# Kernel tuning notes

Hardware: AMD Instinct MI355X
Metric: run time of the kernel (lower is better)

Reference implementation:

```python
import jax, jax.numpy as jnp
import numpy as np
import math

EMBD_SIZE = 1024
OUT_SIZE = 1024
B, N = 8, 2048

def setup_inputs() -> dict:
    key = jax.random.key(0)
    k1, k2, k3 = jax.random.split(key, 3)
    embd = jax.random.normal(k1, (B, N, EMBD_SIZE), dtype=jnp.float32)
    # nn.Linear(embd_size, out_size): weight [out, in], bias [out]
    bound = 1.0 / math.sqrt(EMBD_SIZE)
    W = jax.random.uniform(k2, (OUT_SIZE, EMBD_SIZE), dtype=jnp.float32, minval=-bound, maxval=bound)
    b = jax.random.uniform(k3, (OUT_SIZE,), dtype=jnp.float32, minval=-bound, maxval=bound)
    return {"embd": embd, "W": W, "b": b}

def reference(embd, W, b):
    # c = Linear(embd): [B, N, out_size]
    c = jnp.einsum('bne,oe->bno', embd, W) + b
    # scores = c @ c^T / sqrt(embd_size), softmax over last dim
    score = jnp.einsum('bno,bmo->bnm', c, c) / jnp.sqrt(jnp.float32(EMBD_SIZE))
    score = jax.nn.softmax(score, axis=-1)
    # output = score @ c : [B, N, out_size]
    return jnp.einsum('bnm,bmo->bno', score, c)
```

## Files before the change

### kernel.cpp

```cpp
#include <hip/hip_runtime.h>

typedef unsigned short u16;
typedef unsigned int u32;
typedef __attribute__((ext_vector_type(8))) short short8;
typedef __attribute__((ext_vector_type(4))) float f32x4;

__device__ inline u16 f2bf(float f) {
  u32 x = __float_as_uint(f);
  x += 0x7fff + ((x >> 16) & 1);
  return (u16)(x >> 16);
}
__device__ inline float bf2f(u16 h) {
  return __uint_as_float(((u32)h) << 16);
}
__device__ inline void gload16(const void* g, void* l) {
  __builtin_amdgcn_global_load_lds((const __attribute__((address_space(1))) u32*)g,
                                   (__attribute__((address_space(3))) u32*)l, 16, 0, 0);
}

__device__ inline int sg(int r) {
  return ((r >> 3) & 7) ^ (((r >> 2) & 1) << 2) ^ (((r >> 3) & 1) << 1);
}
__device__ inline int stile_off(int rl, int cl) {
  return rl * 128 + (((cl >> 3) ^ sg(rl)) << 3) + (cl & 7);
}

__global__ void cast_all(const float* __restrict__ embd, const float* __restrict__ W,
                         u16* __restrict__ embd_b, u16* __restrict__ W_b) {
  const float* src; u16* dst; size_t i;
  if (blockIdx.x < 16384) {
    src = embd; dst = embd_b;
    i = ((size_t)blockIdx.x * 256 + threadIdx.x) * 4;
  } else {
    src = W; dst = W_b;
    i = ((size_t)(blockIdx.x - 16384) * 256 + threadIdx.x) * 4;
  }
  float4 v = *(const float4*)(src + i);
  ushort4 o;
  o.x = f2bf(v.x); o.y = f2bf(v.y); o.z = f2bf(v.z); o.w = f2bf(v.w);
  *(ushort4*)(dst + i) = o;
}

#define BM 128
#define BN 128
#define BK 64

template<int MODE>
__global__ __launch_bounds__(256, 2)
void gemm_nt(const u16* __restrict__ A, const u16* __restrict__ B,
             float* __restrict__ Cf, u16* __restrict__ Cb, u16* __restrict__ CT,
             const float* __restrict__ bias, float* __restrict__ rowsum,
             int M, int N, int K, float scale, long sA, long sB, long sC)
{
  __shared__ __align__(16) char smem[32768];
  u16* As = (u16*)smem;
  u16* Bs = As + BM * BK;
  u16* stile = (u16*)smem;
  float* stf = (float*)smem;

  int z, mBase, nBase, bi = 0, bj = 0;
  if (MODE == 0) {
    z = 0;
    mBase = blockIdx.y * BM;
    nBase = blockIdx.x * BN;
  } else if (MODE == 1) {
    z = blockIdx.x;
    int t = blockIdx.y, row = 0;
    const int nb = N >> 7;
    while (t >= nb - row) { t -= nb - row; ++row; }
    bi = row; bj = row + t;
    mBase = bi * BM; nBase = bj * BN;
  } else {
    z = blockIdx.x;
    nBase = (blockIdx.y & 7) * BN;
    mBase = (blockIdx.y >> 3) * BM;
  }

  A += (size_t)z * sA;
  B += (size_t)z * sB;
  if (MODE == 2) Cf += (size_t)z * sC; else Cb += (size_t)z * sC;
  if (MODE != 0) rowsum += (size_t)z * M;

  const int tid  = threadIdx.x;
  const int lane = tid & 63;
  const int wave = tid >> 6;
  const int wm = (wave >> 1) * 64;
  const int wn = (wave & 1) * 64;
  const int q = lane >> 4;
  const int r = lane & 15;
  const int rswz = r & 7;

  const int srow = tid >> 3;
  const int scol = ((tid & 7) ^ (srow & 7)) * 8;
  const int lds0 = tid * 16;

  const u16* a0 = A + (size_t)(mBase + srow) * K + scol;
  const u16* b0 = B + (size_t)(nBase + srow) * K + scol;

  f32x4 acc[4][4] = {};

  for (int k0 = 0; k0 < K; k0 += BK) {
#pragma unroll
    for (int i = 0; i < 4; ++i)
      gload16(a0 + (size_t)(32 * i) * K + k0, (char*)As + lds0 + i * 4096);
#pragma unroll
    for (int i = 0; i < 4; ++i)
      gload16(b0 + (size_t)(32 * i) * K + k0, (char*)Bs + lds0 + i * 4096);
    __syncthreads();

#pragma unroll
    for (int kk = 0; kk < 2; ++kk) {
      short8 af[4], bfr[4];
#pragma unroll
      for (int t = 0; t < 4; ++t) {
        const int go = (((kk * 4 + q) ^ rswz)) * 8;
        af[t]  = *(const short8*)(As + (wm + t * 16 + r) * BK + go);
        bfr[t] = *(const short8*)(Bs + (wn + t * 16 + r) * BK + go);
      }
#pragma unroll
      for (int mi = 0; mi < 4; ++mi)
#pragma unroll
        for (int ni = 0; ni < 4; ++ni)
          acc[mi][ni] = __builtin_amdgcn_mfma_f32_16x16x32_bf16(af[mi], bfr[ni], acc[mi][ni], 0, 0, 0);
    }
    __syncthreads();
  }


  if (MODE == 0) {
    float bv[4];
#pragma unroll
    for (int ni = 0; ni < 4; ++ni) bv[ni] = bias[nBase + wn + ni * 16 + r];
#pragma unroll
    for (int mi = 0; mi < 4; ++mi)
#pragma unroll
      for (int ni = 0; ni < 4; ++ni)
#pragma unroll
        for (int reg = 0; reg < 4; ++reg) {
          int rl = wm + mi * 16 + q * 4 + reg;
          int cl = wn + ni * 16 + r;
          stile[stile_off(rl, cl)] = f2bf(acc[mi][ni][reg] + bv[ni]);
        }
    __syncthreads();
    {
      const int z1 = mBase >> 11;
      const int n0 = mBase & 2047;
      u16* ctb = CT + (size_t)z1 * 1024 * 2048;
#pragma unroll
      for (int rnd = 0; rnd < 8; ++rnd) {
        int idx = rnd * 256 + tid;
        int ch = idx & 15, n = idx >> 4;
        short8 v = *(const short8*)(stile + n * 128 + ((ch ^ sg(n)) << 3));
        *(short8*)(Cb + (size_t)(mBase + n) * N + nBase + ch * 8) = v;
      }
#pragma unroll
      for (int rnd = 0; rnd < 8; ++rnd) {
        int idx = rnd * 256 + tid;
        int ch = idx & 15, cc = idx >> 4;
        short8 v;
#pragma unroll
        for (int j = 0; j < 8; ++j) v[j] = (short)stile[stile_off(ch * 8 + j, cc)];
        *(short8*)(ctb + (size_t)(nBase + cc) * 2048 + n0 + ch * 8) = v;
      }
    }
  } else if (MODE == 1) {
    const bool mirror = (bi != bj);
    float colacc[4] = {0.f, 0.f, 0.f, 0.f};
#pragma unroll
    for (int mi = 0; mi < 4; ++mi) {
      float rs[4] = {0.f, 0.f, 0.f, 0.f};
#pragma unroll
      for (int ni = 0; ni < 4; ++ni)
#pragma unroll
        for (int reg = 0; reg < 4; ++reg) {
          float e = __expf(acc[mi][ni][reg] * scale);
          u16 h = f2bf(e);
          float f = bf2f(h);
          rs[reg] += f;
          if (mirror) colacc[ni] += f;
          stile[stile_off(wm + mi * 16 + q * 4 + reg, wn + ni * 16 + r)] = h;
        }
#pragma unroll
      for (int reg = 0; reg < 4; ++reg) {
        float v = rs[reg];
        v += __shfl_xor(v, 1);
        v += __shfl_xor(v, 2);
        v += __shfl_xor(v, 4);
        v += __shfl_xor(v, 8);
        if (r == 0)
          atomicAdd(&rowsum[mBase + wm + mi * 16 + q * 4 + reg], v);
      }
    }
    if (mirror) {
#pragma unroll
      for (int ni = 0; ni < 4; ++ni) {
        float v = colacc[ni];
        v += __shfl_xor(v, 16);
        v += __shfl_xor(v, 32);
        if (q == 0)
          atomicAdd(&rowsum[nBase + wn + ni * 16 + r], v);
      }
    }
    __syncthreads();
#pragma unroll
    for (int rnd = 0; rnd < 8; ++rnd) {
      int idx = rnd * 256 + tid;
      int ch = idx & 15, n = idx >> 4;
      short8 v = *(const short8*)(stile + n * 128 + ((ch ^ sg(n)) << 3));
      *(short8*)(Cb + (size_t)(mBase + n) * N + nBase + ch * 8) = v;
    }
    if (mirror) {
#pragma unroll
      for (int rnd = 0; rnd < 8; ++rnd) {
        int idx = rnd * 256 + tid;
        int ch = idx & 15, cc = idx >> 4;
        short8 v;
#pragma unroll
        for (int j = 0; j < 8; ++j) v[j] = (short)stile[stile_off(ch * 8 + j, cc)];
        *(short8*)(Cb + (size_t)(nBase + cc) * N + mBase + ch * 8) = v;
      }
    }
  } else {
#pragma unroll
    for (int p = 0; p < 2; ++p) {
      if ((wave >> 1) == p) {
#pragma unroll
        for (int mi = 0; mi < 4; ++mi)
#pragma unroll
          for (int reg = 0; reg < 4; ++reg) {
            int lr = mi * 16 + q * 4 + reg;
            float inv = 1.0f / rowsum[mBase + wm + lr];
#pragma unroll
            for (int ni = 0; ni < 4; ++ni)
              stf[lr * 128 + wn + ni * 16 + r] = acc[mi][ni][reg] * inv;
          }
      }
      __syncthreads();
#pragma unroll
      for (int rnd = 0; rnd < 8; ++rnd) {
        int idx = rnd * 256 + tid;
        int n = idx >> 5, ch = idx & 31;
        float4 v = *(const float4*)(stf + n * 128 + ch * 4);
        *(float4*)(Cf + (size_t)(mBase + p * 64 + n) * N + nBase + ch * 4) = v;
      }
      __syncthreads();
    }
  }
}

extern "C" void kernel_launch(void* const* d_in, const int* in_sizes, int n_in,
                              void* d_out, int out_size, void* d_ws, size_t ws_size,
                              hipStream_t stream) {
  const float* embd = (const float*)d_in[0];
  const float* W    = (const float*)d_in[1];
  const float* bias = (const float*)d_in[2];
  float* out = (float*)d_out;

  char* ws = (char*)d_ws;
  u16* P_b    = (u16*)(ws + 0);
  u16* embd_b = (u16*)(ws + 0);
  u16* W_b    = (u16*)(ws + 33554432);
  u16* c_b    = (u16*)(ws + 67108864);
  u16* cT_b   = (u16*)(ws + 100663296);
  float* rowsum = (float*)(ws + 134217728);

  cast_all<<<17408, 256, 0, stream>>>(embd, W, embd_b, W_b);

  gemm_nt<0><<<dim3(8, 128, 1), 256, 0, stream>>>(
      embd_b, W_b, nullptr, c_b, cT_b, bias, nullptr,
      16384, 1024, 1024, 0.f, 0, 0, 0);

  hipMemsetAsync(rowsum, 0, 16384 * sizeof(float), stream);

  gemm_nt<1><<<dim3(8, 136, 1), 256, 0, stream>>>(
      c_b, c_b, nullptr, P_b, nullptr, nullptr, rowsum,
      2048, 2048, 1024, 0.03125f, 2048L * 1024, 2048L * 1024, 2048L * 2048);

  gemm_nt<2><<<dim3(8, 128, 1), 256, 0, stream>>>(
      P_b, cT_b, out, nullptr, nullptr, nullptr, rowsum,
      2048, 1024, 2048, 0.f, 2048L * 2048, 2048L * 1024, 2048L * 1024);
}
```

Before: 294.8 us.

## Replace PV GEMM with 256x256-tile 512-thread double-buffered kernel

Adds a dedicated P·V kernel that gives each block a 256x256 output tile with 8 waves, loads directly from global memory into a double-buffered 128KB LDS staging area, and prefetches two K-steps ahead. The normalized fp32 output is written directly from registers, where the old version staged it through shared memory. The larger tile raises data reuse per load and cuts the grid from 1024 blocks to 256. The tradeoffs are high LDS and register use, which limits occupancy, and uncoalesced per-lane scalar stores.

```diff
diff --git a/kernel.cpp b/kernel.cpp
--- a/kernel.cpp
+++ b/kernel.cpp
@@ -56,29 +56,24 @@
   u16* As = (u16*)smem;
   u16* Bs = As + BM * BK;
   u16* stile = (u16*)smem;
-  float* stf = (float*)smem;
 
   int z, mBase, nBase, bi = 0, bj = 0;
   if (MODE == 0) {
     z = 0;
     mBase = blockIdx.y * BM;
     nBase = blockIdx.x * BN;
-  } else if (MODE == 1) {
+  } else {
     z = blockIdx.x;
     int t = blockIdx.y, row = 0;
     const int nb = N >> 7;
     while (t >= nb - row) { t -= nb - row; ++row; }
     bi = row; bj = row + t;
     mBase = bi * BM; nBase = bj * BN;
-  } else {
-    z = blockIdx.x;
-    nBase = (blockIdx.y & 7) * BN;
-    mBase = (blockIdx.y >> 3) * BM;
   }
 
   A += (size_t)z * sA;
   B += (size_t)z * sB;
-  if (MODE == 2) Cf += (size_t)z * sC; else Cb += (size_t)z * sC;
+  Cb += (size_t)z * sC;
   if (MODE != 0) rowsum += (size_t)z * M;
 
   const int tid  = threadIdx.x;
@@ -163,7 +158,7 @@
         *(short8*)(ctb + (size_t)(nBase + cc) * 2048 + n0 + ch * 8) = v;
       }
     }
-  } else if (MODE == 1) {
+  } else {
     const bool mirror = (bi != bj);
     float colacc[4] = {0.f, 0.f, 0.f, 0.f};
 #pragma unroll
@@ -220,32 +215,116 @@
         *(short8*)(Cb + (size_t)(nBase + cc) * N + mBase + ch * 8) = v;
       }
     }
-  } else {
-#pragma unroll
-    for (int p = 0; p < 2; ++p) {
-      if ((wave >> 1) == p) {
+  }
+}
+
+#define STAGE_PV(buf, t) do {                                          \
+    const u16* _a = a0 + (size_t)(t) * 64;                             \
+    const u16* _b = b0 + (size_t)(t) * 64;                             \
+    char* _l = (char*)ldsm + (buf) * 65536 + tid * 16;                 \
+    gload16(_a,                      _l);                              \
+    gload16(_a +  64 * (size_t)K,    _l + 8192);                       \
+    gload16(_a + 128 * (size_t)K,    _l + 16384);                      \
+    gload16(_a + 192 * (size_t)K,    _l + 24576);                      \
+    gload16(_b,                      _l + 32768);                      \
+    gload16(_b +  64 * (size_t)K,    _l + 40960);                      \
+    gload16(_b + 128 * (size_t)K,    _l + 49152);                      \
+    gload16(_b + 192 * (size_t)K,    _l + 57344);                      \
+  } while (0)
+
+__global__ __launch_bounds__(512, 2)
+void gemm_pv8(const u16* __restrict__ A, const u16* __restrict__ B,
+              float* __restrict__ Cf, const float* __restrict__ rowsum,
+              int K, int Nn, long sA, long sB, long sC, int Mrs)
+{
+  __shared__ __align__(16) u16 ldsm[65536];
+
+  const int z = blockIdx.x;
+  const int y = blockIdx.y;
+  const int mBase = (y >> 2) * 256;
+  const int nBase = (y & 3) * 256;
+
+  A += (size_t)z * sA;
+  B += (size_t)z * sB;
+  Cf += (size_t)z * sC;
+  rowsum += (size_t)z * Mrs;
+
+  const int tid  = threadIdx.x;
+  const int lane = tid & 63;
+  const int wave = tid >> 6;
+  const int wm = (wave >> 2) * 128;
+  const int wn = (wave & 3) * 64;
+  const int q = lane >> 4;
+  const int r = lane & 15;
+  const int rx = r & 7;
+
+  const int srow = tid >> 3;
+  const int sg8  = ((tid & 7) ^ (srow & 7)) * 8;
+  const u16* a0 = A + (size_t)(mBase + srow) * K + sg8;
+  const u16* b0 = B + (size_t)(nBase + srow) * K + sg8;
+
+  const int NT = K >> 6;
+  const int rA = (wm + r) * 64;
+  const int rB = (wn + r) * 64;
+
+  f32x4 acc[8][4] = {};
+
+  STAGE_PV(0, 0);
+  STAGE_PV(1, 1);
+  asm volatile("s_waitcnt vmcnt(8)" ::: "memory");
+  __builtin_amdgcn_s_barrier();
+
+  for (int i = 0; i < NT; ++i) {
+    const int d = i & 1;
+    const u16* Ab = ldsm + d * 32768;
+    const u16* Bb = Ab + 16384;
+
+#pragma unroll
+    for (int kk = 0; kk < 2; ++kk) {
+      const int gq = ((kk * 4 + q) ^ rx) * 8;
+      short8 bfr[4];
+#pragma unroll
+      for (int t = 0; t < 4; ++t)
+        bfr[t] = *(const short8*)(Bb + rB + t * 1024 + gq);
+#pragma unroll
+      for (int mh = 0; mh < 2; ++mh) {
+        short8 af[4];
+#pragma unroll
+        for (int t = 0; t < 4; ++t)
+          af[t] = *(const short8*)(Ab + rA + (mh * 4 + t) * 1024 + gq);
+        __builtin_amdgcn_s_setprio(1);
 #pragma unroll
         for (int mi = 0; mi < 4; ++mi)
 #pragma unroll
-          for (int reg = 0; reg < 4; ++reg) {
-            int lr = mi * 16 + q * 4 + reg;
-            float inv = 1.0f / rowsum[mBase + wm + lr];
-#pragma unroll
-            for (int ni = 0; ni < 4; ++ni)
-              stf[lr * 128 + wn + ni * 16 + r] = acc[mi][ni][reg] * inv;
-          }
-      }
-      __syncthreads();
-#pragma unroll
-      for (int rnd = 0; rnd < 8; ++rnd) {
-        int idx = rnd * 256 + tid;
-        int n = idx >> 5, ch = idx & 31;
-        float4 v = *(const float4*)(stf + n * 128 + ch * 4);
-        *(float4*)(Cf + (size_t)(mBase + p * 64 + n) * N + nBase + ch * 4) = v;
-      }
-      __syncthreads();
-    }
-  }
+          for (int ni = 0; ni < 4; ++ni)
+            acc[mh * 4 + mi][ni] = __builtin_amdgcn_mfma_f32_16x16x32_bf16(
+                af[mi], bfr[ni], acc[mh * 4 + mi][ni], 0, 0, 0);
+        __builtin_amdgcn_s_setprio(0);
+      }
+    }
+
+    __builtin_amdgcn_s_barrier();
+    if (i + 2 < NT) {
+      STAGE_PV(d, i + 2);
+      asm volatile("s_waitcnt vmcnt(8)" ::: "memory");
+    } else {
+      asm volatile("s_waitcnt vmcnt(0)" ::: "memory");
+    }
+    __builtin_amdgcn_s_barrier();
+    __builtin_amdgcn_sched_barrier(0);
+  }
+
+#pragma unroll
+  for (int mi = 0; mi < 8; ++mi)
+#pragma unroll
+    for (int reg = 0; reg < 4; ++reg) {
+      const int row = mBase + wm + mi * 16 + q * 4 + reg;
+      const float inv = 1.0f / rowsum[row];
+      float* crow = Cf + (size_t)row * Nn + nBase + wn + r;
+#pragma unroll
+      for (int ni = 0; ni < 4; ++ni)
+        crow[ni * 16] = acc[mi][ni][reg] * inv;
+    }
 }
 
 extern "C" void kernel_launch(void* const* d_in, const int* in_sizes, int n_in,
@@ -276,7 +355,7 @@
       c_b, c_b, nullptr, P_b, nullptr, nullptr, rowsum,
       2048, 2048, 1024, 0.03125f, 2048L * 1024, 2048L * 1024, 2048L * 2048);
 
-  gemm_nt<2><<<dim3(8, 128, 1), 256, 0, stream>>>(
-      P_b, cT_b, out, nullptr, nullptr, nullptr, rowsum,
-      2048, 1024, 2048, 0.f, 2048L * 2048, 2048L * 1024, 2048L * 1024);
-}
+  gemm_pv8<<<dim3(8, 32, 1), 512, 0, stream>>>(
+      P_b, cT_b, out, rowsum,
+      2048, 1024, 2048L * 2048, 2048L * 1024, 2048L * 1024, 2048);
+}
```

Result: no change. 289.8 us (-1.7%).
